# Performance work log

Measured on AMD Instinct MI355X. Metric: run time of the kernel, lower is better.

## Reference

```python
import jax, jax.numpy as jnp
import numpy as np
import math
from itertools import permutations

B, C_IN, C_OUT, K, N, D, F_DIM = 2, 4, 8, 4, 224, 2, 128


def _make_perms(k):
    # [k!, k, k] permutation matrices, same ordering as itertools.permutations
    nP = math.factorial(k)
    perms = np.zeros((nP, k, k), dtype=np.float32)
    for c, p in enumerate(permutations(range(k))):
        perms[c, np.arange(k), np.array(p)] = 1.0
    return jnp.asarray(perms)


def setup_inputs() -> dict:
    key = jax.random.key(0)
    ks = jax.random.split(key, 6)
    graph = jax.random.normal(ks[0], (B, C_IN, N, N), jnp.float32)
    types = jax.random.normal(ks[1], (B, C_IN, N), jnp.float32)
    features = jax.random.normal(ks[2], (B, N, F_DIM), jnp.float32)
    # xavier-uniform-ish scales for the learned kernels
    k_struct = jax.random.normal(ks[3], (C_OUT, C_IN, K, K), jnp.float32) * 0.3
    k_row = jax.random.normal(ks[4], (C_OUT, C_IN, K), jnp.float32) * 0.5
    k_col = jax.random.normal(ks[5], (C_OUT, C_IN, K), jnp.float32) * 0.5
    return {"graph": graph, "types": types, "features": features,
            "k_struct": k_struct, "k_row": k_row, "k_col": k_col}


def _forward(graph, types, features, k_struct, k_row, k_col):
    Bn, C, Nn, _ = graph.shape
    k = k_struct.shape[-1]
    new_k = (k - 1) * D + 1
    nH = Nn - new_k + 1            # square graph -> nW == nH
    n_sub = nH * nH
    idx = jnp.arange(nH)[:, None] + jnp.arange(k) * D  # [nH, k] dilated window indices

    # --- _prepare: dilated subgraph extraction (vectorized gather) ---
    g = graph[:, :, idx, :]            # [B,C,nH,k,N]
    g = g[..., idx]                    # [B,C,nH,k,nH,k]
    sub = jnp.transpose(g, (0, 2, 4, 1, 3, 5)).reshape(Bn, n_sub, C, k, k)
    rt = jnp.transpose(types[:, :, idx], (0, 2, 1, 3))  # [B,nH,C,k]
    row_t = jnp.broadcast_to(rt[:, :, None], (Bn, nH, nH, C, k)).reshape(Bn, n_sub, C, k)
    col_t = jnp.broadcast_to(rt[:, None, :], (Bn, nH, nH, C, k)).reshape(Bn, n_sub, C, k)
    rf = features[:, idx, :].sum(axis=-2)              # [B,nH,F]
    feats = rf[:, :, None, :] + rf[:, None, :, :]      # row_features + col_features
    h_mean = feats.reshape(Bn, n_sub, -1).mean(axis=1)  # [B,F]

    # --- permuted kernels ---
    perms = _make_perms(k)                                  # [P,k,k]
    Kp = jnp.einsum('pau,oiuv,pbv->oipab', perms, k_struct, perms)  # P K P^T
    Rp = jnp.einsum('pau,oiu->oipa', perms, k_row)
    Cp = jnp.einsum('pau,oiu->oipa', perms, k_col)

    subf = sub.reshape(-1, C, k, k)   # [n,i,a,b], n = B*n_sub
    rtf = row_t.reshape(-1, C, k)
    ctf = col_t.reshape(-1, C, k)

    # ||X - Y||_F^2 = ||X||^2 + ||Y||^2 - 2<X,Y>, avoids the huge broadcasted diff
    def sq_dist(x2_ni, y2_opi, cross_nopi):
        return y2_opi[None] + x2_ni[:, None, None, :] - 2.0 * cross_nopi

    G2 = jnp.sum(subf * subf, axis=(-2, -1))                       # [n,i]
    K2 = jnp.transpose(jnp.sum(Kp * Kp, axis=(-2, -1)), (0, 2, 1))  # [o,p,i]
    struct = sq_dist(G2, K2, jnp.einsum('niab,oipab->nopi', subf, Kp))
    R2 = jnp.transpose(jnp.sum(Rp * Rp, axis=-1), (0, 2, 1))
    rsim = sq_dist(jnp.sum(rtf * rtf, axis=-1), R2, jnp.einsum('nia,oipa->nopi', rtf, Rp))
    C2 = jnp.transpose(jnp.sum(Cp * Cp, axis=-1), (0, 2, 1))
    csim = sq_dist(jnp.sum(ctf * ctf, axis=-1), C2, jnp.einsum('nia,oipa->nopi', ctf, Cp))

    total = struct + rsim + csim            # [n, o, P, i]
    # maxpool over P of (-total), negated back == min over permutations of total
    pooled = jnp.min(total, axis=2)         # [n, o, i]
    sims = jnp.transpose(pooled.reshape(Bn, n_sub, -1), (0, 2, 1))  # [B, o*i, n_sub]
    out_sim = (1.0 - jax.nn.softmax(sims, axis=-1)) / sims.shape[-1]
    return h_mean, out_sim


def reference(graph, types, features, k_struct, k_row, k_col):
    return _forward(graph, types, features, k_struct, k_row, k_col)
```

## Files before the change

kernel.cpp:

```cpp
#include <hip/hip_runtime.h>
#include <hip/hip_bf16.h>

#define B_    2
#define CIN   4
#define COUT  8
#define KK    4
#define DD    2
#define NN    224
#define FDIM  128
#define NH    218
#define NSUB  (NH*NH)
#define NPERM 24
#define NROWS (B_*COUT*CIN)
#define NSUB4 (NSUB/4)
#define CH4   512
#define MB    ((NSUB4 + CH4 - 1) / CH4)
#define NEGBIG (-3.4e38f)
#define NCOL  192
#define MTILE 128
#define NBLK  ((NSUB + MTILE - 1) / MTILE)
#define STR   40

typedef short short8 __attribute__((ext_vector_type(8)));
typedef float f32x4 __attribute__((ext_vector_type(4)));
typedef unsigned short ushort_t;

__device__ static constexpr int PERM[NPERM][4] = {
  {0,1,2,3},{0,1,3,2},{0,2,1,3},{0,2,3,1},{0,3,1,2},{0,3,2,1},
  {1,0,2,3},{1,0,3,2},{1,2,0,3},{1,2,3,0},{1,3,0,2},{1,3,2,0},
  {2,0,1,3},{2,0,3,1},{2,1,0,3},{2,1,3,0},{2,3,0,1},{2,3,1,0},
  {3,0,1,2},{3,0,2,1},{3,1,0,2},{3,1,2,0},{3,2,0,1},{3,2,1,0}
};

__device__ __forceinline__ void bf16split(float v, ushort_t* h, ushort_t* l) {
  __hip_bfloat16 hh = __float2bfloat16(v);
  float hf = __bfloat162float(hh);
  __hip_bfloat16 ll = __float2bfloat16(v - hf);
  *h = *(const ushort_t*)&hh;
  *l = *(const ushort_t*)&ll;
}

__global__ __launch_bounds__(256) void prep_kernel(
    const float* __restrict__ ks, const float* __restrict__ kr,
    const float* __restrict__ kc, ushort_t* __restrict__ BTgHi,
    ushort_t* __restrict__ BTgLo, float* __restrict__ K2g)
{
  int t = threadIdx.x;
  for (int idx = t; idx < CIN * NCOL; idx += 256) {
    int ci = idx / NCOL, col = idx - ci * NCOL;
    int p = col >> 3, o = col & 7;
    int oc = o * CIN + ci;
    const int* pr = PERM[p];
    float vals[32];
#pragma unroll
    for (int a = 0; a < 4; ++a) {
#pragma unroll
      for (int bb = 0; bb < 4; ++bb)
        vals[a * 4 + bb] = ks[oc * 16 + pr[a] * 4 + pr[bb]];
      vals[16 + a] = kr[oc * 4 + pr[a]];
      vals[20 + a] = kc[oc * 4 + pr[a]];
    }
#pragma unroll
    for (int u = 24; u < 32; ++u) vals[u] = 0.f;
    ushort_t* dh = BTgHi + idx * 32;
    ushort_t* dl = BTgLo + idx * 32;
#pragma unroll
    for (int u = 0; u < 32; ++u) bf16split(vals[u], dh + u, dl + u);
  }
  if (t < 32) {
    int ci = t >> 3, o = t & 7, oc = o * CIN + ci;
    float s2 = 0.f;
#pragma unroll
    for (int u = 0; u < 16; ++u) s2 += ks[oc * 16 + u] * ks[oc * 16 + u];
#pragma unroll
    for (int u = 0; u < 4; ++u)
      s2 += kr[oc * 4 + u] * kr[oc * 4 + u] + kc[oc * 4 + u] * kc[oc * 4 + u];
    K2g[t] = s2;
  }
}

__global__ __launch_bounds__(64) void hmean_kernel(const float* __restrict__ features,
                                                   float* __restrict__ out) {
  int bf = blockIdx.x;
  int b = bf / FDIM, f = bf - b * FDIM;
  int lane = threadIdx.x;
  const float* fb = features + (size_t)b * NN * FDIM + f;
  float acc = 0.f;
  for (int r = lane; r < NN; r += 64) {
    int w = 0;
#pragma unroll
    for (int a = 0; a < KK; ++a) {
      int i0 = r - a * DD;
      if (0 <= i0 && i0 < NH) w++;
    }
    acc += (float)w * fb[(size_t)r * FDIM];
  }
#pragma unroll
  for (int off = 32; off > 0; off >>= 1) acc += __shfl_down(acc, off, 64);
  if (lane == 0) out[bf] = acc * (2.0f / (float)NH);
}

__global__ __launch_bounds__(256, 2) void sims_mfma_kernel(
    const float* __restrict__ graph, const float* __restrict__ types,
    const ushort_t* __restrict__ BTgHi, const ushort_t* __restrict__ BTgLo,
    const float* __restrict__ K2g, float* __restrict__ simsOut)
{
  __shared__ ushort_t lsAhi[MTILE * STR];
  __shared__ ushort_t lsAlo[MTILE * STR];
  __shared__ ushort_t lsBThi[NCOL * STR];
  __shared__ ushort_t lsBTlo[NCOL * STR];
  __shared__ float lsBase[MTILE];
  __shared__ float lsK2[8];

  int t = threadIdx.x;
  int s_base = blockIdx.x * MTILE;
  int b = blockIdx.y;
  int wv = t >> 6, lane = t & 63;
  int c16 = lane & 15, quad = lane >> 4;

#pragma unroll 1
  for (int ci = 0; ci < CIN; ++ci) {
    __syncthreads();
    if (t < 128) {
      int r = t;
      int s = s_base + r;
      float xv[24];
      if (s < NSUB) {
        int ii = s / NH, jj = s - ii * NH;
        const float* gi = graph + (size_t)(b * CIN + ci) * NN * NN;
        const float* ti = types + (size_t)(b * CIN + ci) * NN;
        float bsum = 0.f;
#pragma unroll
        for (int a = 0; a < 4; ++a) {
          const float* row = gi + (size_t)(ii + a * DD) * NN + jj;
#pragma unroll
          for (int bb = 0; bb < 4; ++bb) {
            float v = row[bb * DD];
            xv[a * 4 + bb] = v;
            bsum += v * v;
          }
          float rv = ti[ii + a * DD];
          float cv = ti[jj + a * DD];
          xv[16 + a] = rv; xv[20 + a] = cv;
          bsum += rv * rv + cv * cv;
        }
        lsBase[r] = bsum;
      } else {
#pragma unroll
        for (int u = 0; u < 24; ++u) xv[u] = 0.f;
        lsBase[r] = 0.f;
      }
      ushort_t* ah = lsAhi + r * STR;
      ushort_t* al = lsAlo + r * STR;
#pragma unroll
      for (int u = 0; u < 24; ++u) bf16split(xv[u], ah + u, al + u);
#pragma unroll
      for (int u = 24; u < 32; ++u) { ah[u] = 0; al[u] = 0; }
      if (t < 8) lsK2[t] = K2g[ci * 8 + t];
    } else {
      int tt = t - 128;
      const ushort_t* srcH = BTgHi + ci * (NCOL * 32);
      const ushort_t* srcL = BTgLo + ci * (NCOL * 32);
#pragma unroll
      for (int i = tt; i < NCOL * 4; i += 128) {
        int col = i >> 2, part = i & 3;
        *(short8*)(lsBThi + col * STR + part * 8) = *(const short8*)(srcH + i * 8);
        *(short8*)(lsBTlo + col * STR + part * 8) = *(const short8*)(srcL + i * 8);
      }
    }
    __syncthreads();

    float mx[2][4];
#pragma unroll
    for (int m2 = 0; m2 < 2; ++m2)
#pragma unroll
      for (int rr = 0; rr < 4; ++rr) mx[m2][rr] = NEGBIG;

#pragma unroll 1
    for (int half = 0; half < 2; ++half) {
      short8 bh[6], bl[6];
#pragma unroll
      for (int j = 0; j < 6; ++j) {
        int col = (half * 6 + j) * 16 + c16;
        bh[j] = *(const short8*)(lsBThi + col * STR + quad * 8);
        bl[j] = *(const short8*)(lsBTlo + col * STR + quad * 8);
      }
#pragma unroll
      for (int m2 = 0; m2 < 2; ++m2) {
        int mt = wv * 2 + m2;
        int arow = mt * 16 + c16;
        short8 ah = *(const short8*)(lsAhi + arow * STR + quad * 8);
        short8 al = *(const short8*)(lsAlo + arow * STR + quad * 8);
#pragma unroll
        for (int j = 0; j < 6; ++j) {
          f32x4 c = {0.f, 0.f, 0.f, 0.f};
          c = __builtin_amdgcn_mfma_f32_16x16x32_bf16(ah, bh[j], c, 0, 0, 0);
          c = __builtin_amdgcn_mfma_f32_16x16x32_bf16(ah, bl[j], c, 0, 0, 0);
          c = __builtin_amdgcn_mfma_f32_16x16x32_bf16(al, bh[j], c, 0, 0, 0);
#pragma unroll
          for (int rr = 0; rr < 4; ++rr) mx[m2][rr] = fmaxf(mx[m2][rr], c[rr]);
        }
      }
    }

    int o = lane & 7;
    float k2o = lsK2[o];
    bool writer = (lane & 8) == 0;
#pragma unroll
    for (int m2 = 0; m2 < 2; ++m2) {
      int mt = wv * 2 + m2;
#pragma unroll
      for (int rr = 0; rr < 4; ++rr) {
        float v = mx[m2][rr];
        v = fmaxf(v, __shfl_xor(v, 8, 64));
        int m = mt * 16 + quad * 4 + rr;
        int s = s_base + m;
        if (writer && s < NSUB) {
          float val = lsBase[m] + k2o - 2.0f * v;
          simsOut[(size_t)((b * COUT + o) * CIN + ci) * NSUB + s] = val;
        }
      }
    }
  }
}

__global__ __launch_bounds__(256) void softmax_partial(const float* __restrict__ sims,
                                                       float* __restrict__ partial) {
  int ch = blockIdx.x, row = blockIdx.y;
  int base4 = ch * CH4;
  int n4 = NSUB4 - base4; if (n4 > CH4) n4 = CH4;
  const float4* rp = (const float4*)(sims + (size_t)row * NSUB) + base4;
  int t = threadIdx.x;
  int wave = t >> 6, lane = t & 63;

  float4 a0, a1;
  bool h0 = (t < n4), h1 = (t + 256 < n4);
  if (h0) a0 = rp[t];
  if (h1) a1 = rp[t + 256];

  float m = NEGBIG;
  if (h0) m = fmaxf(fmaxf(a0.x, a0.y), fmaxf(a0.z, a0.w));
  if (h1) m = fmaxf(m, fmaxf(fmaxf(a1.x, a1.y), fmaxf(a1.z, a1.w)));
#pragma unroll
  for (int off = 32; off > 0; off >>= 1) m = fmaxf(m, __shfl_down(m, off, 64));
  __shared__ float red[8];
  if (lane == 0) red[wave] = m;
  __syncthreads();
  float M = fmaxf(fmaxf(red[0], red[1]), fmaxf(red[2], red[3]));

  float e = 0.f;
  if (h0) e  = __expf(a0.x - M) + __expf(a0.y - M) + __expf(a0.z - M) + __expf(a0.w - M);
  if (h1) e += __expf(a1.x - M) + __expf(a1.y - M) + __expf(a1.z - M) + __expf(a1.w - M);
#pragma unroll
  for (int off = 32; off > 0; off >>= 1) e += __shfl_down(e, off, 64);
  if (lane == 0) red[4 + wave] = e;
  __syncthreads();
  if (t == 0) {
    int idx = (row * MB + ch) * 2;
    partial[idx] = M;
    partial[idx + 1] = red[4] + red[5] + red[6] + red[7];
  }
}

__global__ __launch_bounds__(256) void softmax_final(float* __restrict__ sims,
                                                     const float* __restrict__ partial) {
  int ch = blockIdx.x, row = blockIdx.y;
  int t = threadIdx.x;

  __shared__ float sM, sInv;
  if (t < 64) {
    const float* pp = partial + row * MB * 2;
    float m = NEGBIG, l = 0.f;
    if (t < MB) { m = pp[2 * t]; l = pp[2 * t + 1]; }
#pragma unroll
    for (int off = 32; off > 0; off >>= 1) {
      float m2 = __shfl_down(m, off, 64);
      float l2 = __shfl_down(l, off, 64);
      float M = fmaxf(m, m2);
      l = l * __expf(m - M) + l2 * __expf(m2 - M);
      m = M;
    }
    if (t == 0) { sM = m; sInv = 1.0f / l; }
  }
  __syncthreads();
  float M = sM, invS = sInv;

  int base4 = ch * CH4;
  int n4 = NSUB4 - base4; if (n4 > CH4) n4 = CH4;
  float4* rp = (float4*)(sims + (size_t)row * NSUB) + base4;
  const float scale = 1.0f / (float)NSUB;
  for (int i = t; i < n4; i += 256) {
    float4 v = rp[i];
    v.x = (1.0f - __expf(v.x - M) * invS) * scale;
    v.y = (1.0f - __expf(v.y - M) * invS) * scale;
    v.z = (1.0f - __expf(v.z - M) * invS) * scale;
    v.w = (1.0f - __expf(v.w - M) * invS) * scale;
    rp[i] = v;
  }
}

extern "C" void kernel_launch(void* const* d_in, const int* in_sizes, int n_in,
                              void* d_out, int out_size, void* d_ws, size_t ws_size,
                              hipStream_t stream) {
  const float* graph    = (const float*)d_in[0];
  const float* types    = (const float*)d_in[1];
  const float* features = (const float*)d_in[2];
  const float* ks       = (const float*)d_in[3];
  const float* kr       = (const float*)d_in[4];
  const float* kc       = (const float*)d_in[5];
  float* out  = (float*)d_out;
  float* sims = out + B_ * FDIM;

  float* partial  = (float*)d_ws;
  ushort_t* BTgHi = (ushort_t*)((char*)d_ws + 16384);
  ushort_t* BTgLo = (ushort_t*)((char*)d_ws + 16384 + 49152);
  float* K2g      = (float*)((char*)d_ws + 16384 + 2 * 49152);

  prep_kernel<<<1, 256, 0, stream>>>(ks, kr, kc, BTgHi, BTgLo, K2g);
  hmean_kernel<<<B_ * FDIM, 64, 0, stream>>>(features, out);
  dim3 ggrid(NBLK, B_);
  sims_mfma_kernel<<<ggrid, 256, 0, stream>>>(graph, types, BTgHi, BTgLo, K2g, sims);
  dim3 pgrid(MB, NROWS);
  softmax_partial<<<pgrid, 256, 0, stream>>>(sims, partial);
  softmax_final<<<pgrid, 256, 0, stream>>>(sims, partial);
}
```

Baseline: 106.8 us.

## Split input channels across grid blocks and parallelize kernel-prep over blocks

The MFMA sims kernel now gives each input channel its own block (grid y = B*CIN) instead of looping over four channels inside one block. This removes the per-channel barriers, loads the A fragments once, and quadruples the number of blocks, with launch bounds raised to allow 3 blocks per CU. The prep kernel is spread across 4 blocks instead of looping in one block. In exchange, every block reloads the permuted-kernel B tile into LDS, and the higher occupancy target may force register spills.

```diff
diff --git a/kernel.cpp b/kernel.cpp
--- a/kernel.cpp
+++ b/kernel.cpp
@@ -45,9 +45,9 @@
     const float* __restrict__ kc, ushort_t* __restrict__ BTgHi,
     ushort_t* __restrict__ BTgLo, float* __restrict__ K2g)
 {
-  int t = threadIdx.x;
-  for (int idx = t; idx < CIN * NCOL; idx += 256) {
-    int ci = idx / NCOL, col = idx - ci * NCOL;
+  int gid = blockIdx.x * 256 + threadIdx.x;
+  if (gid < CIN * NCOL) {
+    int ci = gid / NCOL, col = gid - ci * NCOL;
     int p = col >> 3, o = col & 7;
     int oc = o * CIN + ci;
     const int* pr = PERM[p];
@@ -62,12 +62,12 @@
     }
 #pragma unroll
     for (int u = 24; u < 32; ++u) vals[u] = 0.f;
-    ushort_t* dh = BTgHi + idx * 32;
-    ushort_t* dl = BTgLo + idx * 32;
+    ushort_t* dh = BTgHi + gid * 32;
+    ushort_t* dl = BTgLo + gid * 32;
 #pragma unroll
     for (int u = 0; u < 32; ++u) bf16split(vals[u], dh + u, dl + u);
-  }
-  if (t < 32) {
+  } else if (gid < CIN * NCOL + 32) {
+    int t = gid - CIN * NCOL;
     int ci = t >> 3, o = t & 7, oc = o * CIN + ci;
     float s2 = 0.f;
 #pragma unroll
@@ -100,7 +100,7 @@
   if (lane == 0) out[bf] = acc * (2.0f / (float)NH);
 }
 
-__global__ __launch_bounds__(256, 2) void sims_mfma_kernel(
+__global__ __launch_bounds__(256, 3) void sims_mfma_kernel(
     const float* __restrict__ graph, const float* __restrict__ types,
     const ushort_t* __restrict__ BTgHi, const ushort_t* __restrict__ BTgLo,
     const float* __restrict__ K2g, float* __restrict__ simsOut)
@@ -114,111 +114,116 @@
 
   int t = threadIdx.x;
   int s_base = blockIdx.x * MTILE;
-  int b = blockIdx.y;
+  int bci = blockIdx.y;
+  int b = bci >> 2, ci = bci & 3;
   int wv = t >> 6, lane = t & 63;
   int c16 = lane & 15, quad = lane >> 4;
 
+  {
+    const ushort_t* srcH = BTgHi + ci * (NCOL * 32);
+    const ushort_t* srcL = BTgLo + ci * (NCOL * 32);
+#pragma unroll
+    for (int i = t; i < 2 * NCOL * 4; i += 256) {
+      int isLo = i >= NCOL * 4;
+      int j = isLo ? i - NCOL * 4 : i;
+      int col = j >> 2, part = j & 3;
+      const ushort_t* src = (isLo ? srcL : srcH) + j * 8;
+      ushort_t* dst = (isLo ? lsBTlo : lsBThi) + col * STR + part * 8;
+      *(short8*)dst = *(const short8*)src;
+    }
+  }
+  if (t < 8) lsK2[t] = K2g[ci * 8 + t];
+
+  if (t < 128) {
+    int r = t;
+    int s = s_base + r;
+    float xv[24];
+    if (s < NSUB) {
+      int ii = s / NH, jj = s - ii * NH;
+      const float* gi = graph + (size_t)(b * CIN + ci) * NN * NN;
+      const float* ti = types + (size_t)(b * CIN + ci) * NN;
+      float bsum = 0.f;
+#pragma unroll
+      for (int a = 0; a < 4; ++a) {
+        const float* row = gi + (size_t)(ii + a * DD) * NN + jj;
+#pragma unroll
+        for (int bb = 0; bb < 4; ++bb) {
+          float v = row[bb * DD];
+          xv[a * 4 + bb] = v;
+          bsum += v * v;
+        }
+        float rv = ti[ii + a * DD];
+        float cv = ti[jj + a * DD];
+        xv[16 + a] = rv; xv[20 + a] = cv;
+        bsum += rv * rv + cv * cv;
+      }
+      lsBase[r] = bsum;
+    } else {
+#pragma unroll
+      for (int u = 0; u < 24; ++u) xv[u] = 0.f;
+      lsBase[r] = 0.f;
+    }
+    ushort_t* ah = lsAhi + r * STR;
+    ushort_t* al = lsAlo + r * STR;
+#pragma unroll
+    for (int u = 0; u < 24; ++u) bf16split(xv[u], ah + u, al + u);
+#pragma unroll
+    for (int u = 24; u < 32; ++u) { ah[u] = 0; al[u] = 0; }
+  }
+  __syncthreads();
+
+  short8 ah2[2], al2[2];
+#pragma unroll
+  for (int m2 = 0; m2 < 2; ++m2) {
+    int arow = (wv * 2 + m2) * 16 + c16;
+    ah2[m2] = *(const short8*)(lsAhi + arow * STR + quad * 8);
+    al2[m2] = *(const short8*)(lsAlo + arow * STR + quad * 8);
+  }
+
+  float mx[2][4];
+#pragma unroll
+  for (int m2 = 0; m2 < 2; ++m2)
+#pragma unroll
+    for (int rr = 0; rr < 4; ++rr) mx[m2][rr] = NEGBIG;
+
 #pragma unroll 1
-  for (int ci = 0; ci < CIN; ++ci) {
-    __syncthreads();
-    if (t < 128) {
-      int r = t;
-      int s = s_base + r;
-      float xv[24];
-      if (s < NSUB) {
-        int ii = s / NH, jj = s - ii * NH;
-        const float* gi = graph + (size_t)(b * CIN + ci) * NN * NN;
-        const float* ti = types + (size_t)(b * CIN + ci) * NN;
-        float bsum = 0.f;
-#pragma unroll
-        for (int a = 0; a < 4; ++a) {
-          const float* row = gi + (size_t)(ii + a * DD) * NN + jj;
-#pragma unroll
-          for (int bb = 0; bb < 4; ++bb) {
-            float v = row[bb * DD];
-            xv[a * 4 + bb] = v;
-            bsum += v * v;
-          }
-          float rv = ti[ii + a * DD];
-          float cv = ti[jj + a * DD];
-          xv[16 + a] = rv; xv[20 + a] = cv;
-          bsum += rv * rv + cv * cv;
-        }
-        lsBase[r] = bsum;
-      } else {
-#pragma unroll
-        for (int u = 0; u < 24; ++u) xv[u] = 0.f;
-        lsBase[r] = 0.f;
+  for (int half = 0; half < 2; ++half) {
+    short8 bh[6], bl[6];
+#pragma unroll
+    for (int j = 0; j < 6; ++j) {
+      int col = (half * 6 + j) * 16 + c16;
+      bh[j] = *(const short8*)(lsBThi + col * STR + quad * 8);
+      bl[j] = *(const short8*)(lsBTlo + col * STR + quad * 8);
+    }
+#pragma unroll
+    for (int m2 = 0; m2 < 2; ++m2) {
+#pragma unroll
+      for (int j = 0; j < 6; ++j) {
+        f32x4 c = {0.f, 0.f, 0.f, 0.f};
+        c = __builtin_amdgcn_mfma_f32_16x16x32_bf16(ah2[m2], bh[j], c, 0, 0, 0);
+        c = __builtin_amdgcn_mfma_f32_16x16x32_bf16(ah2[m2], bl[j], c, 0, 0, 0);
+        c = __builtin_amdgcn_mfma_f32_16x16x32_bf16(al2[m2], bh[j], c, 0, 0, 0);
+#pragma unroll
+        for (int rr = 0; rr < 4; ++rr) mx[m2][rr] = fmaxf(mx[m2][rr], c[rr]);
       }
-      ushort_t* ah = lsAhi + r * STR;
-      ushort_t* al = lsAlo + r * STR;
-#pragma unroll
-      for (int u = 0; u < 24; ++u) bf16split(xv[u], ah + u, al + u);
-#pragma unroll
-      for (int u = 24; u < 32; ++u) { ah[u] = 0; al[u] = 0; }
-      if (t < 8) lsK2[t] = K2g[ci * 8 + t];
-    } else {
-      int tt = t - 128;
-      const ushort_t* srcH = BTgHi + ci * (NCOL * 32);
-      const ushort_t* srcL = BTgLo + ci * (NCOL * 32);
-#pragma unroll
-      for (int i = tt; i < NCOL * 4; i += 128) {
-        int col = i >> 2, part = i & 3;
-        *(short8*)(lsBThi + col * STR + part * 8) = *(const short8*)(srcH + i * 8);
-        *(short8*)(lsBTlo + col * STR + part * 8) = *(const short8*)(srcL + i * 8);
-      }
-    }
-    __syncthreads();
-
-    float mx[2][4];
-#pragma unroll
-    for (int m2 = 0; m2 < 2; ++m2)
-#pragma unroll
-      for (int rr = 0; rr < 4; ++rr) mx[m2][rr] = NEGBIG;
-
-#pragma unroll 1
-    for (int half = 0; half < 2; ++half) {
-      short8 bh[6], bl[6];
-#pragma unroll
-      for (int j = 0; j < 6; ++j) {
-        int col = (half * 6 + j) * 16 + c16;
-        bh[j] = *(const short8*)(lsBThi + col * STR + quad * 8);
-        bl[j] = *(const short8*)(lsBTlo + col * STR + quad * 8);
-      }
-#pragma unroll
-      for (int m2 = 0; m2 < 2; ++m2) {
-        int mt = wv * 2 + m2;
-        int arow = mt * 16 + c16;
-        short8 ah = *(const short8*)(lsAhi + arow * STR + quad * 8);
-        short8 al = *(const short8*)(lsAlo + arow * STR + quad * 8);
-#pragma unroll
-        for (int j = 0; j < 6; ++j) {
-          f32x4 c = {0.f, 0.f, 0.f, 0.f};
-          c = __builtin_amdgcn_mfma_f32_16x16x32_bf16(ah, bh[j], c, 0, 0, 0);
-          c = __builtin_amdgcn_mfma_f32_16x16x32_bf16(ah, bl[j], c, 0, 0, 0);
-          c = __builtin_amdgcn_mfma_f32_16x16x32_bf16(al, bh[j], c, 0, 0, 0);
-#pragma unroll
-          for (int rr = 0; rr < 4; ++rr) mx[m2][rr] = fmaxf(mx[m2][rr], c[rr]);
-        }
-      }
-    }
-
-    int o = lane & 7;
-    float k2o = lsK2[o];
-    bool writer = (lane & 8) == 0;
-#pragma unroll
-    for (int m2 = 0; m2 < 2; ++m2) {
-      int mt = wv * 2 + m2;
-#pragma unroll
-      for (int rr = 0; rr < 4; ++rr) {
-        float v = mx[m2][rr];
-        v = fmaxf(v, __shfl_xor(v, 8, 64));
-        int m = mt * 16 + quad * 4 + rr;
-        int s = s_base + m;
-        if (writer && s < NSUB) {
-          float val = lsBase[m] + k2o - 2.0f * v;
-          simsOut[(size_t)((b * COUT + o) * CIN + ci) * NSUB + s] = val;
-        }
+    }
+  }
+
+  int o = lane & 7;
+  float k2o = lsK2[o];
+  bool writer = (lane & 8) == 0;
+#pragma unroll
+  for (int m2 = 0; m2 < 2; ++m2) {
+    int mt = wv * 2 + m2;
+#pragma unroll
+    for (int rr = 0; rr < 4; ++rr) {
+      float v = mx[m2][rr];
+      v = fmaxf(v, __shfl_xor(v, 8, 64));
+      int m = mt * 16 + quad * 4 + rr;
+      int s = s_base + m;
+      if (writer && s < NSUB) {
+        float val = lsBase[m] + k2o - 2.0f * v;
+        simsOut[(size_t)((b * COUT + o) * CIN + ci) * NSUB + s] = val;
       }
     }
   }
@@ -316,9 +321,9 @@
   ushort_t* BTgLo = (ushort_t*)((char*)d_ws + 16384 + 49152);
   float* K2g      = (float*)((char*)d_ws + 16384 + 2 * 49152);
 
-  prep_kernel<<<1, 256, 0, stream>>>(ks, kr, kc, BTgHi, BTgLo, K2g);
+  prep_kernel<<<4, 256, 0, stream>>>(ks, kr, kc, BTgHi, BTgLo, K2g);
   hmean_kernel<<<B_ * FDIM, 64, 0, stream>>>(features, out);
-  dim3 ggrid(NBLK, B_);
+  dim3 ggrid(NBLK, B_ * CIN);
   sims_mfma_kernel<<<ggrid, 256, 0, stream>>>(graph, types, BTgHi, BTgLo, K2g, sims);
   dim3 pgrid(MB, NROWS);
   softmax_partial<<<pgrid, 256, 0, stream>>>(sims, partial);
```

New measurement: 105.4 us. About the same (-1.3%).
